# Kernel optimization log

Measured on AMD Instinct MI355X. Metric: run time of the kernel, lower is better.

The kernel has to match this reference:

```python
import jax, jax.numpy as jnp
import numpy as np

NUM_ANGLES = 120
MAX_CONF = 100
FIELD = 50  # prot_field_size L


def setup_inputs() -> dict:
    key = jax.random.key(0)
    ks = jax.random.split(key, 4)
    B = 16
    return {
        "receptor": jax.random.normal(ks[0], (B, 1, FIELD, FIELD), jnp.float32),
        "ligand": jax.random.normal(ks[1], (B, 1, FIELD, FIELD), jnp.float32),
        "w_repr": jax.random.normal(ks[2], (2, 1, 3, 3), jnp.float32) * 0.3,
        "b_repr": jnp.zeros((2,), jnp.float32),
        "w_score": jax.random.normal(ks[3], (1, 4), jnp.float32) * 0.1,
        "b_score": jnp.zeros((1,), jnp.float32),
    }


def reference(receptor, ligand, w_repr, b_repr, w_score, b_score):
    B, _, H, W = receptor.shape  # H = W = FIELD

    # ---- scoring_model.repr : conv(1->2, SAME) + ReLU (stand-in for EQ repr net)
    def repr_net(x):
        y = jax.lax.conv_general_dilated(
            x, w_repr, (1, 1), "SAME", dimension_numbers=("NCHW", "OIHW", "NCHW"))
        return jax.nn.relu(y + b_repr[None, :, None, None])

    rec_feat = repr_net(receptor)  # (B,2,H,W)
    lig_feat = repr_net(ligand)    # (B,2,H,W)

    # ---- rotate: torch affine_grid + grid_sample (bilinear, align_corners=True, zero pad)
    ang = (2.0 * np.pi / NUM_ANGLES) * jnp.arange(NUM_ANGLES, dtype=jnp.float32)
    ca, sa = jnp.cos(ang), jnp.sin(ang)
    lin = jnp.linspace(-1.0, 1.0, H)
    gy, gx = jnp.meshgrid(lin, lin, indexing="ij")  # rows=y, cols=x
    # theta = [[c,-s,0],[s,c,0]] maps output coords -> input coords
    x_in = ca[:, None, None] * gx - sa[:, None, None] * gy  # (A,H,W)
    y_in = sa[:, None, None] * gx + ca[:, None, None] * gy
    px = (x_in + 1.0) * 0.5 * (W - 1)
    py = (y_in + 1.0) * 0.5 * (H - 1)
    x0 = jnp.floor(px).astype(jnp.int32); y0 = jnp.floor(py).astype(jnp.int32)
    x1 = x0 + 1; y1 = y0 + 1
    wx1 = px - x0; wx0 = 1.0 - wx1
    wy1 = py - y0; wy0 = 1.0 - wy1

    def tap(yi, xi, wgt):
        val = lig_feat[:, :, jnp.clip(yi, 0, H - 1), jnp.clip(xi, 0, W - 1)]  # (B,C,A,H,W)
        ok = ((yi >= 0) & (yi < H) & (xi >= 0) & (xi < W)).astype(lig_feat.dtype)
        return val * (wgt * ok)

    lig_rot = (tap(y0, x0, wy0 * wx0) + tap(y0, x1, wy0 * wx1)
               + tap(y1, x0, wy1 * wx0) + tap(y1, x1, wy1 * wx1))
    lig_rot = jnp.transpose(lig_rot, (2, 0, 1, 3, 4))  # (A,B,C,H,W)

    # ---- ProteinConv2D: FFT cross-correlation over all channel pairs, output 2L x 2L
    S = 2 * H
    pad = ((0, 0), (0, 0), (0, H), (0, W))
    Frec = jnp.fft.rfft2(jnp.pad(rec_feat, pad))              # (B,C,S,S/2+1)
    Flig = jnp.fft.rfft2(jnp.pad(lig_rot, ((0, 0),) + pad))   # (A,B,C,S,S/2+1)
    cross = jnp.einsum("bcxy,abdxy->abcdxy", jnp.conj(Frec), Flig)
    A_, C = NUM_ANGLES, rec_feat.shape[1]
    corr = jnp.fft.irfft2(cross.reshape(A_, B, C * C, S, S // 2 + 1), s=(S, S))
    corr = jnp.fft.fftshift(corr, axes=(-2, -1))              # (A,B,4,S,S) centered

    # ---- scoring_model.scorer : Linear(4->1) applied per translation
    scores = jnp.einsum("abcij,c->abij", corr, w_score[0]) + b_score[0]  # (A,B,S,S)

    # ---- update_top: greedy iterative argmin extraction with zero masking
    flat = scores.reshape(A_, B, S * S)

    def greedy(v):
        def step(s, _):
            i = jnp.argmin(s)
            return s.at[i].set(0.0), (i, s[i])
        _, (idx, val) = jax.lax.scan(step, v, None, length=MAX_CONF)
        return idx, val

    idxs, vals = jax.vmap(jax.vmap(greedy))(flat)  # each (A,B,K)

    # ---- final top-1 per batch over all angles/extractions (stable first-min tiebreak)
    K = MAX_CONF
    vals_b = jnp.transpose(vals, (1, 0, 2)).reshape(B, A_ * K)
    j = jnp.argmin(vals_b, axis=1)
    a = j // K
    k = j % K
    pos = idxs[a, jnp.arange(B), k]
    Lf = jnp.float32(S / 2)
    x = (pos // S).astype(jnp.float32)
    y = (pos % S).astype(jnp.float32)
    angles_out = ang[a][:, None]                               # (B,1)
    translations = jnp.stack([x - Lf, y - Lf], axis=1)         # (B,2)
    return angles_out, translations
```

## Files before the change

### kernel.cpp

```cpp
#include <hip/hip_runtime.h>
#include <math.h>

#define NANG 120
#define NB   16
#define H    50
#define SD   100
#define NBIN 51
#define PADB 3
#define BROWS 60
#define BST  106
#define WST  104
#define RTST 52
#define CST  58
#define AX   58

__device__ __align__(16) float g_Arec[NB*2*AX*NBIN*2 + 64];
__device__ __align__(16) float g_ligc[NB*2*H*H];
__device__ __align__(16) float g_W[H*WST];
__device__ __align__(16) float g_P[NBIN*128 + 64];
__device__ float g_resV[NANG*NB];
__device__ int   g_resP[NANG*NB];

__device__ const int g_s3[2][8][2] = {
  {{-5,127},{-9,127},{-13,127},{-17,127},{-21,-49},{-25,-45},{-29,-41},{-33,-37}},
  {{-1,127},{3,47},{7,43},{11,39},{15,35},{19,27},{23,31},{127,127}}
};

__global__ __launch_bounds__(512) void k_prep(const float* __restrict__ rec,
                                              const float* __restrict__ lig,
                                              const float* __restrict__ wr,
                                              const float* __restrict__ br,
                                              const float* __restrict__ wsc) {
  const int blk = blockIdx.x;
  const int tid = threadIdx.x;
  if (blk == NB) {
    for (int u = tid; u < H*WST; u += 512) {
      int y = u / WST, col = u % WST;
      float v = 0.f;
      if (col < 2*NBIN) {
        int om = col >> 1;
        int k = (om * y) % SD;
        double ang = 6.283185307179586 * (double)k / 100.0;
        v = (col & 1) ? (float)(-sin(ang)) : (float)cos(ang);
      }
      g_W[u] = v;
    }
    for (int u = tid; u < NBIN*128; u += 512) {
      int om = u >> 7, q = u & 127;
      int dy = q >> 1;
      float v = 0.f;
      if (dy <= 49) {
        int k = (om * dy) % SD;
        double ang = 6.283185307179586 * (double)k / 100.0;
        v = (q & 1) ? (float)sin(ang) : (float)cos(ang);
      }
      g_P[u] = v;
    }
    return;
  }
  const int b = blk;
  __shared__ float recf[2*H*H];
  __shared__ float tbl[SD*2];
  for (int k = tid; k < SD; k += 512) {
    double ang = 6.283185307179586 * (double)k / 100.0;
    tbl[2*k]   = (float)cos(ang);
    tbl[2*k+1] = (float)sin(ang);
  }
  const float* rimg = rec + b*H*H;
  const float* limg = lig + b*H*H;
  for (int p = tid; p < H*H; p += 512) {
    int i = p / H, j = p - (p/H)*H;
    float ar0 = br[0], ar1 = br[1], al0 = br[0], al1 = br[1];
    for (int di = 0; di < 3; ++di) {
      int ii = i + di - 1;
      if (ii < 0 || ii >= H) continue;
      for (int dj = 0; dj < 3; ++dj) {
        int jj = j + dj - 1;
        if (jj < 0 || jj >= H) continue;
        float rv = rimg[ii*H+jj], lv = limg[ii*H+jj];
        float w0 = wr[di*3 + dj], w1 = wr[9 + di*3 + dj];
        ar0 += w0*rv; ar1 += w1*rv; al0 += w0*lv; al1 += w1*lv;
      }
    }
    ar0 = fmaxf(ar0, 0.f); ar1 = fmaxf(ar1, 0.f);
    al0 = fmaxf(al0, 0.f); al1 = fmaxf(al1, 0.f);
    recf[p] = ar0; recf[H*H + p] = ar1;
    g_ligc[((b*2+0)*H + i)*H + j] = wsc[0]*al0 + wsc[1]*al1;
    g_ligc[((b*2+1)*H + i)*H + j] = wsc[2]*al0 + wsc[3]*al1;
  }
  for (int u = tid; u < 2*8*102; u += 512) {
    int c = u / 816; int r = u % 816;
    int x = 50 + r / 102; int q = r % 102;
    g_Arec[((b*2+c)*AX + x)*102 + q] = 0.f;
  }
  __syncthreads();
  for (int u = tid; u < 2*H*NBIN; u += 512) {
    int om = u % NBIN; int rest = u / NBIN; int x = rest % H; int c = rest / H;
    const float* row = recf + (c*H + x)*H;
    float sr = 0.f, si = 0.f;
    int k = 0;
    for (int y = 0; y < H; ++y) {
      float rv = row[y];
      sr += rv * tbl[2*k];
      si -= rv * tbl[2*k+1];
      k += om; if (k >= SD) k -= SD;
    }
    float* dst = g_Arec + ((b*2+c)*AX + x)*102 + 2*om;
    dst[0] = sr; dst[1] = si;
  }
}

#define P3_STEP(uu) do { \
  float Ar = ar_[(uu)&7], Ai = ai_[(uu)&7]; \
  { const int sl=(uu)&7;     c0 += Ar*br_[sl] + Ai*bi_[sl]; c4 += Ar*bi_[sl] - Ai*br_[sl]; } \
  { const int sl=((uu)+1)&7; c1 += Ar*br_[sl] + Ai*bi_[sl]; c5 += Ar*bi_[sl] - Ai*br_[sl]; } \
  { const int sl=((uu)+2)&7; c2 += Ar*br_[sl] + Ai*bi_[sl]; c6 += Ar*bi_[sl] - Ai*br_[sl]; } \
  { const int sl=((uu)+3)&7; c3 += Ar*br_[sl] + Ai*bi_[sl]; c7 += Ar*bi_[sl] - Ai*br_[sl]; } \
} while(0)

__global__ __launch_bounds__(512, 4) void k_main() {
  const int bid = blockIdx.x;
  const int a = bid % NANG;
  const int b = bid / NANG;
  const int tid = threadIdx.x;

  __shared__ __align__(16) float sMem[18652];
  float* sB = sMem;
  float* Rt = sMem + 12720;
  float* Cr = sMem + 12720;
  float* Ci = sMem + 12720 + NBIN*CST;
  float* sRedV = sMem + 18636;
  int*   sRedP = (int*)(sMem + 18644);

  for (int u = tid; u < 2*10*BST; u += 512) {
    int ch = u / (10*BST);
    int r  = (u % (10*BST)) / BST;
    int col = u % BST;
    int row = (r < 3) ? r : r + 50;
    sB[ch*BROWS*BST + row*BST + col] = 0.f;
  }

  float angf = 0.05235987755982988f * (float)a;
  float ca = cosf(angf), sa = sinf(angf);
  const float* L0 = g_ligc + (b*2+0)*H*H;
  const float* L1 = g_ligc + (b*2+1)*H*H;
  for (int p = tid; p < H*H; p += 512) {
    int i = p / H, j = p - (p/H)*H;
    float gy = -1.f + (float)i*(2.f/49.f);
    float gx = -1.f + (float)j*(2.f/49.f);
    float x_in = ca*gx - sa*gy;
    float y_in = sa*gx + ca*gy;
    float px = (x_in + 1.f)*0.5f*49.f;
    float py = (y_in + 1.f)*0.5f*49.f;
    float fx = floorf(px), fy = floorf(py);
    int x0 = (int)fx, y0 = (int)fy;
    int x1 = x0 + 1, y1 = y0 + 1;
    float wx1 = px - fx, wx0 = 1.f - wx1;
    float wy1 = py - fy, wy0 = 1.f - wy1;
    float v0 = 0.f, v1 = 0.f;
    if (y0 >= 0 && y0 < H) {
      if (x0 >= 0 && x0 < H) { float w = wy0*wx0; int o = y0*H+x0; v0 += w*L0[o]; v1 += w*L1[o]; }
      if (x1 >= 0 && x1 < H) { float w = wy0*wx1; int o = y0*H+x1; v0 += w*L0[o]; v1 += w*L1[o]; }
    }
    if (y1 >= 0 && y1 < H) {
      if (x0 >= 0 && x0 < H) { float w = wy1*wx0; int o = y1*H+x0; v0 += w*L0[o]; v1 += w*L1[o]; }
      if (x1 >= 0 && x1 < H) { float w = wy1*wx1; int o = y1*H+x1; v0 += w*L0[o]; v1 += w*L1[o]; }
    }
    Rt[(0*H + j)*RTST + i] = v0;
    Rt[(1*H + j)*RTST + i] = v1;
  }
  __syncthreads();

  if (tid < 442) {
    int c = tid / 221;
    int r = tid % 221;
    int cg = r % 17;
    int it = r / 17;
    int i0 = it*4;
    int col0 = 6*cg;
    float pacc[4][6];
    #pragma unroll
    for (int p = 0; p < 4; ++p)
      #pragma unroll
      for (int q = 0; q < 6; ++q) pacc[p][q] = 0.f;
    const float* rtc = Rt + c*H*RTST + i0;
    const float* wt = g_W + col0;
    #pragma unroll 2
    for (int y = 0; y < H; ++y) {
      float4 rv = *(const float4*)&rtc[y*RTST];
      float ww[6];
      #pragma unroll
      for (int q = 0; q < 3; ++q) {
        float2 w2 = *(const float2*)&wt[y*WST + 2*q];
        ww[2*q] = w2.x; ww[2*q+1] = w2.y;
      }
      float rr[4] = {rv.x, rv.y, rv.z, rv.w};
      #pragma unroll
      for (int p = 0; p < 4; ++p)
        #pragma unroll
        for (int q = 0; q < 6; ++q) pacc[p][q] += rr[p]*ww[q];
    }
    float* dst = sB + c*BROWS*BST + col0;
    #pragma unroll
    for (int p = 0; p < 4; ++p) {
      int i = i0 + p;
      if (i < H) {
        #pragma unroll
        for (int q = 0; q < 3; ++q) {
          float2 o = {pacc[p][2*q], pacc[p][2*q+1]};
          *(float2*)&dst[(PADB+i)*BST + 2*q] = o;
        }
      }
    }
  }
  __syncthreads();

  const int wid = tid >> 6, lane = tid & 63;
  const int om = (lane <= 50) ? lane : 50;
  const bool omValid = (lane <= 50);
  float bestV = 3.0e38f; int bestP = 0;

  for (int h = 0; h < 2; ++h) {
    const int lagBase = h ? -1 : -49;

    #pragma unroll
    for (int slot = 0; slot < 2; ++slot) {
      const int d0 = g_s3[h][wid][slot];
      if (d0 != 127) {
        const int x_lo = max(0, -(d0+3));
        const int x_hi = min(H, H - d0);
        const int ng = (x_hi - x_lo + 7) >> 3;
        float c0=0,c1=0,c2=0,c3=0,c4=0,c5=0,c6=0,c7=0;
        #pragma unroll 1
        for (int c = 0; c < 2; ++c) {
          const float* Ap = g_Arec + ((b*2+c)*AX + x_lo)*102 + 2*om;
          const float* Bp = sB + c*BROWS*BST + (PADB + x_lo + d0)*BST + 2*om;
          float br_[8], bi_[8], ar_[8], ai_[8];
          #pragma unroll
          for (int s = 0; s < 8; ++s) {
            float2 bv = *(const float2*)&Bp[s*BST];
            br_[s] = bv.x; bi_[s] = bv.y;
            float2 av = *(const float2*)&Ap[s*102];
            ar_[s] = av.x; ai_[s] = av.y;
          }
          #pragma unroll 1
          for (int g = 0; g < ng-1; ++g) {
            #pragma unroll
            for (int u = 0; u < 8; ++u) {
              P3_STEP(u);
              float2 bv = *(const float2*)&Bp[(u+8)*BST];
              br_[u] = bv.x; bi_[u] = bv.y;
              float2 av = *(const float2*)&Ap[(u+8)*102];
              ar_[u] = av.x; ai_[u] = av.y;
            }
            Bp += 8*BST; Ap += 8*102;
          }
          {
            const int rowcap = 56 - (x_lo + 8*(ng-1) + d0);
            P3_STEP(0); P3_STEP(1); P3_STEP(2); P3_STEP(3); P3_STEP(4);
            #pragma unroll
            for (int s = 0; s < 3; ++s) {
              int o = min(8+s, rowcap);
              float2 bv = *(const float2*)&Bp[o*BST];
              br_[s] = bv.x; bi_[s] = bv.y;
            }
            P3_STEP(5); P3_STEP(6); P3_STEP(7);
          }
        }
        if (omValid) {
          const float sc = (om == 0 || om == 50) ? 0.5f : 1.0f;
          int base = om*CST + (d0 - lagBase);
          float2 v0 = {c0*sc, c1*sc}; *(float2*)&Cr[base]   = v0;
          float2 v1 = {c2*sc, c3*sc}; *(float2*)&Cr[base+2] = v1;
          float2 v2 = {c4*sc, c5*sc}; *(float2*)&Ci[base]   = v2;
          float2 v3 = {c6*sc, c7*sc}; *(float2*)&Ci[base+2] = v3;
        }
      }
    }
    __syncthreads();

    {
      const int nLT = h ? 26 : 24;
      const int units = nLT * 17;
      const int gBase = h ? 48 : 0;
      if (tid < units) {
        int lt = tid % nLT;
        int dt = tid / nLT;
        int l0 = 2*lt, dy0 = 3*dt;
        float su[2][3], sv[2][3];
        #pragma unroll
        for (int k = 0; k < 2; ++k)
          #pragma unroll
          for (int j = 0; j < 3; ++j) { su[k][j] = 0.f; sv[k][j] = 0.f; }
        const float* crp = Cr + l0;
        const float* cip = Ci + l0;
        const float* tp = g_P + 2*dy0;
        #pragma unroll 3
        for (int om2 = 0; om2 < NBIN; ++om2) {
          float2 cv = *(const float2*)&crp[om2*CST];
          float2 iv = *(const float2*)&cip[om2*CST];
          float2 t0 = *(const float2*)&tp[om2*128];
          float2 t1 = *(const float2*)&tp[om2*128 + 2];
          float2 t2 = *(const float2*)&tp[om2*128 + 4];
          float cc[2] = {cv.x, cv.y};
          float ii[2] = {iv.x, iv.y};
          float co[3] = {t0.x, t1.x, t2.x};
          float si[3] = {t0.y, t1.y, t2.y};
          #pragma unroll
          for (int k = 0; k < 2; ++k)
            #pragma unroll
            for (int j = 0; j < 3; ++j) {
              su[k][j] += cc[k]*co[j];
              sv[k][j] += ii[k]*si[j];
            }
        }
        #pragma unroll
        for (int k = 0; k < 2; ++k) {
          int lagIdx = gBase + l0 + k;
          if (lagIdx <= 98) {
            int row = lagIdx + 1;
            #pragma unroll
            for (int j = 0; j < 3; ++j) {
              int dy = dy0 + j;
              if (dy <= 49) {
                float vp = su[k][j] - sv[k][j];
                float vm = su[k][j] + sv[k][j];
                int posp = row*SD + (50 + dy);
                int posm = row*SD + (50 - dy);
                if (vp < bestV || (vp == bestV && posp < bestP)) { bestV = vp; bestP = posp; }
                if (vm < bestV || (vm == bestV && posm < bestP)) { bestV = vm; bestP = posm; }
              }
            }
          }
        }
      }
    }
    __syncthreads();
  }

  #pragma unroll
  for (int off = 32; off > 0; off >>= 1) {
    float v2 = __shfl_xor(bestV, off, 64);
    int   p2 = __shfl_xor(bestP, off, 64);
    if (v2 < bestV || (v2 == bestV && p2 < bestP)) { bestV = v2; bestP = p2; }
  }
  if (lane == 0) { sRedV[wid] = bestV; sRedP[wid] = bestP; }
  __syncthreads();
  if (tid == 0) {
    float bv = sRedV[0]; int bp = sRedP[0];
    for (int w = 1; w < 8; ++w) {
      float v2 = sRedV[w]; int p2 = sRedP[w];
      if (v2 < bv || (v2 == bv && p2 < bp)) { bv = v2; bp = p2; }
    }
    g_resV[bid] = bv; g_resP[bid] = bp;
  }
}

__global__ void k_final(float* __restrict__ out) {
  int b = threadIdx.x;
  if (b >= NB) return;
  float bv = 0.f; int bp = 0; int ba = 0;
  for (int a = 0; a < NANG; ++a) {
    float v = g_resV[b*NANG + a];
    if (v < bv) { bv = v; bp = g_resP[b*NANG + a]; ba = a; }
  }
  out[b] = 0.05235987755982988f * (float)ba;
  out[NB + 2*b]     = (float)(bp / SD) - 50.f;
  out[NB + 2*b + 1] = (float)(bp % SD) - 50.f;
}

extern "C" void kernel_launch(void* const* d_in, const int* in_sizes, int n_in,
                              void* d_out, int out_size, void* d_ws, size_t ws_size,
                              hipStream_t stream) {
  const float* rec = (const float*)d_in[0];
  const float* lig = (const float*)d_in[1];
  const float* wr  = (const float*)d_in[2];
  const float* br  = (const float*)d_in[3];
  const float* wsc = (const float*)d_in[4];
  (void)in_sizes; (void)n_in; (void)out_size; (void)d_ws; (void)ws_size;
  hipLaunchKernelGGL(k_prep, dim3(NB+1), dim3(512), 0, stream, rec, lig, wr, br, wsc);
  hipLaunchKernelGGL(k_main, dim3(NANG*NB), dim3(512), 0, stream);
  hipLaunchKernelGGL(k_final, dim3(1), dim3(64), 0, stream, (float*)d_out);
}
```

Baseline: 329.9 us.

## Widen cross-correlation lag tiles to 8 and process channels sequentially in one pass

Each wavefront now computes 8 lags per tile, with 16 accumulators per tile, instead of 4, so each A/B load is reused across twice as many lags. The two lag halves are merged into a single pass, and the final inverse-DFT stage uses 4-lag tiles over all 99 lags at once. The two channels are processed one after the other through a single shared sB buffer, which shrinks shared memory, but this adds a synchronisation per channel. Register pressure rises from 32 accumulators per thread and the new lane layout may raise VGPR use, which could reduce occupancy under the (512,4) launch bounds.

```diff
diff --git a/kernel.cpp b/kernel.cpp
--- a/kernel.cpp
+++ b/kernel.cpp
@@ -6,12 +6,12 @@
 #define H    50
 #define SD   100
 #define NBIN 51
-#define PADB 3
-#define BROWS 60
+#define PADB 7
+#define BROWS 72
 #define BST  106
 #define WST  104
 #define RTST 52
-#define CST  58
+#define CLAG 104
 #define AX   58
 
 __device__ __align__(16) float g_Arec[NB*2*AX*NBIN*2 + 64];
@@ -21,9 +21,8 @@
 __device__ float g_resV[NANG*NB];
 __device__ int   g_resP[NANG*NB];
 
-__device__ const int g_s3[2][8][2] = {
-  {{-5,127},{-9,127},{-13,127},{-17,127},{-21,-49},{-25,-45},{-29,-41},{-33,-37}},
-  {{-1,127},{3,47},{7,43},{11,39},{15,35},{19,27},{23,31},{127,127}}
+__device__ const int g_s8[8][2] = {
+  {-1,127},{-9,-49},{7,47},{-17,-41},{15,39},{-25,-33},{23,31},{127,127}
 };
 
 __global__ __launch_bounds__(512) void k_prep(const float* __restrict__ rec,
@@ -110,13 +109,52 @@
   }
 }
 
-#define P3_STEP(uu) do { \
+#define STEP8(uu) do { \
   float Ar = ar_[(uu)&7], Ai = ai_[(uu)&7]; \
-  { const int sl=(uu)&7;     c0 += Ar*br_[sl] + Ai*bi_[sl]; c4 += Ar*bi_[sl] - Ai*br_[sl]; } \
-  { const int sl=((uu)+1)&7; c1 += Ar*br_[sl] + Ai*bi_[sl]; c5 += Ar*bi_[sl] - Ai*br_[sl]; } \
-  { const int sl=((uu)+2)&7; c2 += Ar*br_[sl] + Ai*bi_[sl]; c6 += Ar*bi_[sl] - Ai*br_[sl]; } \
-  { const int sl=((uu)+3)&7; c3 += Ar*br_[sl] + Ai*bi_[sl]; c7 += Ar*bi_[sl] - Ai*br_[sl]; } \
+  _Pragma("unroll") \
+  for (int k = 0; k < 8; ++k) { \
+    const int sl = ((uu)+k)&7; \
+    acc[2*k]   += Ar*br_[sl] + Ai*bi_[sl]; \
+    acc[2*k+1] += Ar*bi_[sl] - Ai*br_[sl]; \
+  } \
 } while(0)
+
+__device__ __forceinline__ void p3_tile8(int d0, int b, int c, const float* sB, int om,
+                                         float (&acc)[16]) {
+  const int x_lo = max(0, -(d0+7));
+  const int x_hi = min(H, H - d0);
+  const int ng = (x_hi - x_lo + 7) >> 3;
+  const float* Ap = g_Arec + ((b*2+c)*AX + x_lo)*102 + 2*om;
+  const float* Bp = sB + (PADB + x_lo + d0)*BST + 2*om;
+  float br_[8], bi_[8], ar_[8], ai_[8];
+  #pragma unroll
+  for (int s = 0; s < 8; ++s) {
+    float2 bv = *(const float2*)&Bp[s*BST];
+    br_[s] = bv.x; bi_[s] = bv.y;
+    float2 av = *(const float2*)&Ap[s*102];
+    ar_[s] = av.x; ai_[s] = av.y;
+  }
+  #pragma unroll 1
+  for (int g = 0; g < ng-1; ++g) {
+    #pragma unroll
+    for (int u = 0; u < 8; ++u) {
+      STEP8(u);
+      float2 bv = *(const float2*)&Bp[(u+8)*BST];
+      br_[u] = bv.x; bi_[u] = bv.y;
+      float2 av = *(const float2*)&Ap[(u+8)*102];
+      ar_[u] = av.x; ai_[u] = av.y;
+    }
+    Bp += 8*BST; Ap += 8*102;
+  }
+  #pragma unroll
+  for (int u = 0; u < 8; ++u) {
+    STEP8(u);
+    if (u < 7) {
+      float2 bv = *(const float2*)&Bp[(u+8)*BST];
+      br_[u] = bv.x; bi_[u] = bv.y;
+    }
+  }
+}
 
 __global__ __launch_bounds__(512, 4) void k_main() {
   const int bid = blockIdx.x;
@@ -124,20 +162,19 @@
   const int b = bid / NANG;
   const int tid = threadIdx.x;
 
-  __shared__ __align__(16) float sMem[18652];
-  float* sB = sMem;
-  float* Rt = sMem + 12720;
-  float* Cr = sMem + 12720;
-  float* Ci = sMem + 12720 + NBIN*CST;
-  float* sRedV = sMem + 18636;
-  int*   sRedP = (int*)(sMem + 18644);
-
-  for (int u = tid; u < 2*10*BST; u += 512) {
-    int ch = u / (10*BST);
-    int r  = (u % (10*BST)) / BST;
-    int col = u % BST;
-    int row = (r < 3) ? r : r + 50;
-    sB[ch*BROWS*BST + row*BST + col] = 0.f;
+  __shared__ __align__(16) float sMem[18256];
+  float* sB  = sMem;
+  float* Rt0 = sMem + 7632;
+  float* Rt1 = sMem + 7632 + 2600;
+  float* Cr  = sMem + 7632;
+  float* Ci  = sMem + 7632 + NBIN*CLAG;
+  float* sRedV = sMem + 18240;
+  int*   sRedP = (int*)(sMem + 18248);
+
+  for (int u = tid; u < 22*BST; u += 512) {
+    int r = u / BST;
+    int row = (r < PADB) ? r : r + 50;
+    sB[row*BST + (u % BST)] = 0.f;
   }
 
   float angf = 0.05235987755982988f * (float)a;
@@ -166,45 +203,54 @@
       if (x0 >= 0 && x0 < H) { float w = wy1*wx0; int o = y1*H+x0; v0 += w*L0[o]; v1 += w*L1[o]; }
       if (x1 >= 0 && x1 < H) { float w = wy1*wx1; int o = y1*H+x1; v0 += w*L0[o]; v1 += w*L1[o]; }
     }
-    Rt[(0*H + j)*RTST + i] = v0;
-    Rt[(1*H + j)*RTST + i] = v1;
+    Rt0[j*RTST + i] = v0;
+    Rt1[j*RTST + i] = v1;
   }
   __syncthreads();
 
-  if (tid < 442) {
-    int c = tid / 221;
-    int r = tid % 221;
-    int cg = r % 17;
-    int it = r / 17;
-    int i0 = it*4;
-    int col0 = 6*cg;
-    float pacc[4][6];
-    #pragma unroll
-    for (int p = 0; p < 4; ++p)
+  const int wid = tid >> 6, lane = tid & 63;
+  const int om = (lane <= 50) ? lane : 50;
+  const bool omValid = (lane <= 50);
+  const int d0A = g_s8[wid][0];
+  const int d0B = g_s8[wid][1];
+
+  float accA[16], accB[16];
+  #pragma unroll
+  for (int k = 0; k < 16; ++k) { accA[k] = 0.f; accB[k] = 0.f; }
+
+  #pragma unroll 1
+  for (int c = 0; c < 2; ++c) {
+    if (tid < 425) {
+      int cg = tid % 17;
+      int rt = tid / 17;
+      int i0 = 2*rt;
+      int col0 = 6*cg;
+      float pacc[2][6];
       #pragma unroll
-      for (int q = 0; q < 6; ++q) pacc[p][q] = 0.f;
-    const float* rtc = Rt + c*H*RTST + i0;
-    const float* wt = g_W + col0;
-    #pragma unroll 2
-    for (int y = 0; y < H; ++y) {
-      float4 rv = *(const float4*)&rtc[y*RTST];
-      float ww[6];
+      for (int p = 0; p < 2; ++p)
+        #pragma unroll
+        for (int q = 0; q < 6; ++q) pacc[p][q] = 0.f;
+      const float* rtc = (c ? Rt1 : Rt0) + i0;
+      const float* wt = g_W + col0;
+      #pragma unroll 2
+      for (int y = 0; y < H; ++y) {
+        float2 rv = *(const float2*)&rtc[y*RTST];
+        float ww[6];
+        #pragma unroll
+        for (int q = 0; q < 3; ++q) {
+          float2 w2 = *(const float2*)&wt[y*WST + 2*q];
+          ww[2*q] = w2.x; ww[2*q+1] = w2.y;
+        }
+        float rr[2] = {rv.x, rv.y};
+        #pragma unroll
+        for (int p = 0; p < 2; ++p)
+          #pragma unroll
+          for (int q = 0; q < 6; ++q) pacc[p][q] += rr[p]*ww[q];
+      }
+      float* dst = sB + col0;
       #pragma unroll
-      for (int q = 0; q < 3; ++q) {
-        float2 w2 = *(const float2*)&wt[y*WST + 2*q];
-        ww[2*q] = w2.x; ww[2*q+1] = w2.y;
-      }
-      float rr[4] = {rv.x, rv.y, rv.z, rv.w};
-      #pragma unroll
-      for (int p = 0; p < 4; ++p)
-        #pragma unroll
-        for (int q = 0; q < 6; ++q) pacc[p][q] += rr[p]*ww[q];
-    }
-    float* dst = sB + c*BROWS*BST + col0;
-    #pragma unroll
-    for (int p = 0; p < 4; ++p) {
-      int i = i0 + p;
-      if (i < H) {
+      for (int p = 0; p < 2; ++p) {
+        int i = i0 + p;
         #pragma unroll
         for (int q = 0; q < 3; ++q) {
           float2 o = {pacc[p][2*q], pacc[p][2*q+1]};
@@ -212,130 +258,87 @@
         }
       }
     }
+    __syncthreads();
+
+    if (d0A != 127) p3_tile8(d0A, b, c, sB, om, accA);
+    if (d0B != 127) p3_tile8(d0B, b, c, sB, om, accB);
+    __syncthreads();
+  }
+
+  if (omValid) {
+    const float sc = (om == 0 || om == 50) ? 0.5f : 1.0f;
+    if (d0A != 127) {
+      int base = om*CLAG + (d0A + 49);
+      float4 v0 = {accA[0]*sc, accA[2]*sc, accA[4]*sc, accA[6]*sc};
+      float4 v1 = {accA[8]*sc, accA[10]*sc, accA[12]*sc, accA[14]*sc};
+      float4 w0 = {accA[1]*sc, accA[3]*sc, accA[5]*sc, accA[7]*sc};
+      float4 w1 = {accA[9]*sc, accA[11]*sc, accA[13]*sc, accA[15]*sc};
+      *(float4*)&Cr[base] = v0; *(float4*)&Cr[base+4] = v1;
+      *(float4*)&Ci[base] = w0; *(float4*)&Ci[base+4] = w1;
+    }
+    if (d0B != 127) {
+      int base = om*CLAG + (d0B + 49);
+      float4 v0 = {accB[0]*sc, accB[2]*sc, accB[4]*sc, accB[6]*sc};
+      float4 v1 = {accB[8]*sc, accB[10]*sc, accB[12]*sc, accB[14]*sc};
+      float4 w0 = {accB[1]*sc, accB[3]*sc, accB[5]*sc, accB[7]*sc};
+      float4 w1 = {accB[9]*sc, accB[11]*sc, accB[13]*sc, accB[15]*sc};
+      *(float4*)&Cr[base] = v0; *(float4*)&Cr[base+4] = v1;
+      *(float4*)&Ci[base] = w0; *(float4*)&Ci[base+4] = w1;
+    }
   }
   __syncthreads();
 
-  const int wid = tid >> 6, lane = tid & 63;
-  const int om = (lane <= 50) ? lane : 50;
-  const bool omValid = (lane <= 50);
   float bestV = 3.0e38f; int bestP = 0;
-
-  for (int h = 0; h < 2; ++h) {
-    const int lagBase = h ? -1 : -49;
-
+  if (tid < 442) {
+    int lt = tid % 26;
+    int dt = tid / 26;
+    int l0 = 4*lt, dy0 = 3*dt;
+    float su[4][3], sv[4][3];
     #pragma unroll
-    for (int slot = 0; slot < 2; ++slot) {
-      const int d0 = g_s3[h][wid][slot];
-      if (d0 != 127) {
-        const int x_lo = max(0, -(d0+3));
-        const int x_hi = min(H, H - d0);
-        const int ng = (x_hi - x_lo + 7) >> 3;
-        float c0=0,c1=0,c2=0,c3=0,c4=0,c5=0,c6=0,c7=0;
-        #pragma unroll 1
-        for (int c = 0; c < 2; ++c) {
-          const float* Ap = g_Arec + ((b*2+c)*AX + x_lo)*102 + 2*om;
-          const float* Bp = sB + c*BROWS*BST + (PADB + x_lo + d0)*BST + 2*om;
-          float br_[8], bi_[8], ar_[8], ai_[8];
-          #pragma unroll
-          for (int s = 0; s < 8; ++s) {
-            float2 bv = *(const float2*)&Bp[s*BST];
-            br_[s] = bv.x; bi_[s] = bv.y;
-            float2 av = *(const float2*)&Ap[s*102];
-            ar_[s] = av.x; ai_[s] = av.y;
-          }
-          #pragma unroll 1
-          for (int g = 0; g < ng-1; ++g) {
-            #pragma unroll
-            for (int u = 0; u < 8; ++u) {
-              P3_STEP(u);
-              float2 bv = *(const float2*)&Bp[(u+8)*BST];
-              br_[u] = bv.x; bi_[u] = bv.y;
-              float2 av = *(const float2*)&Ap[(u+8)*102];
-              ar_[u] = av.x; ai_[u] = av.y;
-            }
-            Bp += 8*BST; Ap += 8*102;
-          }
-          {
-            const int rowcap = 56 - (x_lo + 8*(ng-1) + d0);
-            P3_STEP(0); P3_STEP(1); P3_STEP(2); P3_STEP(3); P3_STEP(4);
-            #pragma unroll
-            for (int s = 0; s < 3; ++s) {
-              int o = min(8+s, rowcap);
-              float2 bv = *(const float2*)&Bp[o*BST];
-              br_[s] = bv.x; bi_[s] = bv.y;
-            }
-            P3_STEP(5); P3_STEP(6); P3_STEP(7);
+    for (int k = 0; k < 4; ++k)
+      #pragma unroll
+      for (int j = 0; j < 3; ++j) { su[k][j] = 0.f; sv[k][j] = 0.f; }
+    const float* crp = Cr + l0;
+    const float* cip = Ci + l0;
+    const float* tp = g_P + 2*dy0;
+    #pragma unroll 3
+    for (int om2 = 0; om2 < NBIN; ++om2) {
+      float4 c4 = *(const float4*)&crp[om2*CLAG];
+      float4 i4 = *(const float4*)&cip[om2*CLAG];
+      float2 t0 = *(const float2*)&tp[om2*128];
+      float2 t1 = *(const float2*)&tp[om2*128 + 2];
+      float2 t2 = *(const float2*)&tp[om2*128 + 4];
+      float cc[4] = {c4.x, c4.y, c4.z, c4.w};
+      float ii[4] = {i4.x, i4.y, i4.z, i4.w};
+      float co[3] = {t0.x, t1.x, t2.x};
+      float si[3] = {t0.y, t1.y, t2.y};
+      #pragma unroll
+      for (int k = 0; k < 4; ++k)
+        #pragma unroll
+        for (int j = 0; j < 3; ++j) {
+          su[k][j] += cc[k]*co[j];
+          sv[k][j] += ii[k]*si[j];
+        }
+    }
+    #pragma unroll
+    for (int k = 0; k < 4; ++k) {
+      int lagIdx = l0 + k;
+      if (lagIdx <= 98) {
+        int row = lagIdx + 1;
+        #pragma unroll
+        for (int j = 0; j < 3; ++j) {
+          int dy = dy0 + j;
+          if (dy <= 49) {
+            float vp = su[k][j] - sv[k][j];
+            float vm = su[k][j] + sv[k][j];
+            int posp = row*SD + (50 + dy);
+            int posm = row*SD + (50 - dy);
+            if (vp < bestV || (vp == bestV && posp < bestP)) { bestV = vp; bestP = posp; }
+            if (vm < bestV || (vm == bestV && posm < bestP)) { bestV = vm; bestP = posm; }
           }
         }
-        if (omValid) {
-          const float sc = (om == 0 || om == 50) ? 0.5f : 1.0f;
-          int base = om*CST + (d0 - lagBase);
-          float2 v0 = {c0*sc, c1*sc}; *(float2*)&Cr[base]   = v0;
-          float2 v1 = {c2*sc, c3*sc}; *(float2*)&Cr[base+2] = v1;
-          float2 v2 = {c4*sc, c5*sc}; *(float2*)&Ci[base]   = v2;
-          float2 v3 = {c6*sc, c7*sc}; *(float2*)&Ci[base+2] = v3;
-        }
-      }
-    }
-    __syncthreads();
-
-    {
-      const int nLT = h ? 26 : 24;
-      const int units = nLT * 17;
-      const int gBase = h ? 48 : 0;
-      if (tid < units) {
-        int lt = tid % nLT;
-        int dt = tid / nLT;
-        int l0 = 2*lt, dy0 = 3*dt;
-        float su[2][3], sv[2][3];
-        #pragma unroll
-        for (int k = 0; k < 2; ++k)
-          #pragma unroll
-          for (int j = 0; j < 3; ++j) { su[k][j] = 0.f; sv[k][j] = 0.f; }
-        const float* crp = Cr + l0;
-        const float* cip = Ci + l0;
-        const float* tp = g_P + 2*dy0;
-        #pragma unroll 3
-        for (int om2 = 0; om2 < NBIN; ++om2) {
-          float2 cv = *(const float2*)&crp[om2*CST];
-          float2 iv = *(const float2*)&cip[om2*CST];
-          float2 t0 = *(const float2*)&tp[om2*128];
-          float2 t1 = *(const float2*)&tp[om2*128 + 2];
-          float2 t2 = *(const float2*)&tp[om2*128 + 4];
-          float cc[2] = {cv.x, cv.y};
-          float ii[2] = {iv.x, iv.y};
-          float co[3] = {t0.x, t1.x, t2.x};
-          float si[3] = {t0.y, t1.y, t2.y};
-          #pragma unroll
-          for (int k = 0; k < 2; ++k)
-            #pragma unroll
-            for (int j = 0; j < 3; ++j) {
-              su[k][j] += cc[k]*co[j];
-              sv[k][j] += ii[k]*si[j];
-            }
-        }
-        #pragma unroll
-        for (int k = 0; k < 2; ++k) {
-          int lagIdx = gBase + l0 + k;
-          if (lagIdx <= 98) {
-            int row = lagIdx + 1;
-            #pragma unroll
-            for (int j = 0; j < 3; ++j) {
-              int dy = dy0 + j;
-              if (dy <= 49) {
-                float vp = su[k][j] - sv[k][j];
-                float vm = su[k][j] + sv[k][j];
-                int posp = row*SD + (50 + dy);
-                int posm = row*SD + (50 - dy);
-                if (vp < bestV || (vp == bestV && posp < bestP)) { bestV = vp; bestP = posp; }
-                if (vm < bestV || (vm == bestV && posm < bestP)) { bestV = vm; bestP = posm; }
-              }
-            }
-          }
-        }
-      }
-    }
-    __syncthreads();
+      }
+    }
   }
 
   #pragma unroll
```

Result: slower. 390.9 us (+18.5%).
